# Kernel tuning notes

Measured on AMD Instinct MI355X. Metric: run time of the kernel, lower is better.

The kernel has to match this reference:

```python
import jax, jax.numpy as jnp
import numpy as np

EMBED_DIM = 1024
N_HEADS = 16
HEAD_DIM = EMBED_DIM // N_HEADS


def setup_inputs() -> dict:
    key = jax.random.key(0)
    ks = jax.random.split(key, 9)
    s = 1.0 / np.sqrt(EMBED_DIM)
    x = jax.random.normal(ks[0], (4, 2048, EMBED_DIM), dtype=jnp.float32)
    Wq = jax.random.uniform(ks[1], (EMBED_DIM, EMBED_DIM), jnp.float32, -s, s)
    bq = jax.random.uniform(ks[2], (EMBED_DIM,), jnp.float32, -s, s)
    Wk = jax.random.uniform(ks[3], (EMBED_DIM, EMBED_DIM), jnp.float32, -s, s)
    bk = jax.random.uniform(ks[4], (EMBED_DIM,), jnp.float32, -s, s)
    Wv = jax.random.uniform(ks[5], (EMBED_DIM, EMBED_DIM), jnp.float32, -s, s)
    bv = jax.random.uniform(ks[6], (EMBED_DIM,), jnp.float32, -s, s)
    Wo = jax.random.uniform(ks[7], (EMBED_DIM, EMBED_DIM), jnp.float32, -s, s)
    bo = jax.random.uniform(ks[8], (EMBED_DIM,), jnp.float32, -s, s)
    return {"x": x, "Wq": Wq, "bq": bq, "Wk": Wk, "bk": bk,
            "Wv": Wv, "bv": bv, "Wo": Wo, "bo": bo}


def reference(x, Wq, bq, Wk, bk, Wv, bv, Wo, bo):
    B, S, _ = x.shape
    # projections (PyTorch Linear: x @ W.T + b; weights stored as [in,out] here)
    q = x @ Wq + bq
    k = x @ Wk + bk
    v = x @ Wv + bv
    # [B, H, S, D]
    q = q.reshape(B, S, N_HEADS, HEAD_DIM).transpose(0, 2, 1, 3)
    k = k.reshape(B, S, N_HEADS, HEAD_DIM).transpose(0, 2, 1, 3)
    v = v.reshape(B, S, N_HEADS, HEAD_DIM).transpose(0, 2, 1, 3)
    scores = jnp.einsum('bhsd,bhtd->bhst', q, k) / np.sqrt(HEAD_DIM).astype(np.float32)
    attn = jax.nn.softmax(scores, axis=-1)
    out = jnp.einsum('bhst,bhtd->bhsd', attn, v)
    out = out.transpose(0, 2, 1, 3).reshape(B, S, EMBED_DIM)
    return out @ Wo + bo  # dropout=0 (eval) -> identity
```

## Files before the change

### kernel.cpp

```cpp
#include <hip/hip_runtime.h>
#include <stdint.h>

#define EMBED 1024
#define NH 16
#define HD 64
#define SEQ 2048
#define BATCH 4
#define M_TOT (BATCH*SEQ)
#define QSCALE 0.18033688011112042f

typedef __attribute__((ext_vector_type(8))) short short8;
typedef __attribute__((ext_vector_type(4))) float floatx4;
typedef __attribute__((ext_vector_type(4))) unsigned int uintx4;

__device__ __forceinline__ unsigned short f2bf(float f) {
    union { float f; unsigned int u; } v; v.f = f;
    unsigned int r = v.u + 0x7fffu + ((v.u >> 16) & 1u);
    return (unsigned short)(r >> 16);
}

__device__ __forceinline__ void load_lds16(const unsigned short* g, unsigned short* l) {
    __builtin_amdgcn_global_load_lds(
        (const __attribute__((address_space(1))) unsigned int*)g,
        (__attribute__((address_space(3))) unsigned int*)l, 16, 0, 0);
}

__global__ void cvt_x(const float* __restrict__ x, unsigned short* __restrict__ xb) {
    int i = (blockIdx.x * 256 + threadIdx.x) * 4;
    float4 v = *(const float4*)(x + i);
    ushort4 o;
    o.x = f2bf(v.x); o.y = f2bf(v.y); o.z = f2bf(v.z); o.w = f2bf(v.w);
    *(ushort4*)(xb + i) = o;
}

__global__ void wtrans(const float* __restrict__ w0, const float* __restrict__ w1,
                       const float* __restrict__ w2, const float* __restrict__ w3,
                       unsigned short* __restrict__ t0, unsigned short* __restrict__ t1,
                       unsigned short* __restrict__ t2, unsigned short* __restrict__ t3) {
    __shared__ float tile[32][33];
    const float* W; unsigned short* T;
    switch (blockIdx.z) { case 0: W=w0; T=t0; break; case 1: W=w1; T=t1; break;
                          case 2: W=w2; T=t2; break; default: W=w3; T=t3; }
    int n0 = blockIdx.x * 32, k0 = blockIdx.y * 32;
    int tx = threadIdx.x, ty = threadIdx.y;
    #pragma unroll
    for (int i = 0; i < 4; i++)
        tile[ty + i*8][tx] = W[(k0 + ty + i*8) * EMBED + n0 + tx];
    __syncthreads();
    #pragma unroll
    for (int i = 0; i < 4; i++)
        T[(n0 + ty + i*8) * EMBED + k0 + tx] = f2bf(tile[tx][ty + i*8]);
}

#define GBUFS 8192

template<bool STG, int WAITN>
__device__ __forceinline__ void ktile(int t,
        const unsigned short* Abase, const unsigned short* Bbase,
        const unsigned short* Asrc, const unsigned short* Bsrc,
        unsigned short* sda, unsigned short* sdb, floatx4 (&acc)[4][2]) {
    const int bo = (t & 3) * GBUFS;
    short8 fA[4], fB[2];
    #pragma unroll
    for (int m=0;m<4;m++) fA[m] = *(const short8*)(Abase + bo + m*512);
    #pragma unroll
    for (int n=0;n<2;n++) fB[n] = *(const short8*)(Bbase + bo + n*512);
    if (STG) {
        const int buf_ = (t+3) & 3; const int ko_ = (t+3)*32;
        load_lds16(Asrc + ko_, sda + buf_*GBUFS);
        load_lds16(Bsrc + ko_, sdb + buf_*GBUFS);
    }
    #pragma unroll
    for (int m=0;m<4;m++)
      #pragma unroll
      for (int n=0;n<2;n++)
        acc[m][n] = __builtin_amdgcn_mfma_f32_16x16x32_bf16(fA[m], fB[n], acc[m][n], 0,0,0);
    if (WAITN == 4)      { asm volatile("s_waitcnt vmcnt(4)" ::: "memory"); asm volatile("s_barrier" ::: "memory"); }
    else if (WAITN == 2) { asm volatile("s_waitcnt vmcnt(2)" ::: "memory"); asm volatile("s_barrier" ::: "memory"); }
    else if (WAITN == 0) { asm volatile("s_waitcnt vmcnt(0)" ::: "memory"); asm volatile("s_barrier" ::: "memory"); }
}

template<int MODE>
__global__ __launch_bounds__(512, 4) void gemmk(
        const unsigned short* __restrict__ A, const unsigned short* __restrict__ BT,
        const float* __restrict__ b0, const float* __restrict__ b1, const float* __restrict__ b2,
        void* __restrict__ o0, void* __restrict__ o1, void* __restrict__ o2) {
    constexpr int BM = 128, BN = 128;
    __shared__ unsigned short lds[4*GBUFS];
    const int tid = threadIdx.x;
    const int lane = tid & 63, wave = tid >> 6;
    const int quad = lane >> 4, l16 = lane & 15;
    const int wm = wave >> 2, wn = wave & 3;
    const int id = blockIdx.x;
    constexpr int MS = (M_TOT/BM)/8;
    const int xcd = id & 7, j = id >> 3;
    const int mblk = (xcd * MS + (j % MS)) * BM;
    const int nblk = (j / MS) * BN;

    const int srow = tid >> 2;
    const int scol = ((tid & 3) ^ (srow & 3) ^ ((srow >> 2) & 3)) * 8;
    const unsigned short* Asrc = A  + (size_t)(mblk + srow) * EMBED + scol;
    const unsigned short* Bsrc = BT + (size_t)(nblk + srow) * EMBED + scol;
    unsigned short* sda = lds + wave * 512;
    unsigned short* sdb = lds + BM*32 + wave * 512;

    const int cs = (quad ^ (l16 & 3) ^ ((l16 >> 2) & 3)) * 8;
    const unsigned short* Abase = lds + (wm*64 + l16)*32 + cs;
    const unsigned short* Bbase = lds + BM*32 + (wn*32 + l16)*32 + cs;

    floatx4 acc[4][2];
    #pragma unroll
    for (int m=0;m<4;m++)
      #pragma unroll
      for (int n=0;n<2;n++) acc[m][n] = (floatx4){0.f,0.f,0.f,0.f};

    #pragma unroll
    for (int p=0;p<3;p++) {
        load_lds16(Asrc + p*32, sda + p*GBUFS);
        load_lds16(Bsrc + p*32, sdb + p*GBUFS);
    }
    asm volatile("s_waitcnt vmcnt(4)" ::: "memory");
    asm volatile("s_barrier" ::: "memory");

    #pragma unroll 4
    for (int t = 0; t < 28; ++t)
        ktile<true,4>(t, Abase, Bbase, Asrc, Bsrc, sda, sdb, acc);
    ktile<true, 4>(28, Abase, Bbase, Asrc, Bsrc, sda, sdb, acc);
    ktile<false,2>(29, Abase, Bbase, Asrc, Bsrc, sda, sdb, acc);
    ktile<false,0>(30, Abase, Bbase, Asrc, Bsrc, sda, sdb, acc);
    ktile<false,-1>(31, Abase, Bbase, Asrc, Bsrc, sda, sdb, acc);

    if constexpr (MODE == 1) {
        float* O = (float*)o0;
        #pragma unroll
        for (int mt=0;mt<4;mt++)
          #pragma unroll
          for (int nt=0;nt<2;nt++) {
            int col = nblk + wn*32 + nt*16 + l16;
            float bv = b0[col];
            #pragma unroll
            for (int r=0;r<4;r++) {
                int row = mblk + wm*64 + mt*16 + quad*4 + r;
                O[(size_t)row * EMBED + col] = acc[mt][nt][r] + bv;
            }
          }
    } else {
        int which = nblk >> 10;
        const float* bs = (which==0) ? b0 : (which==1) ? b1 : b2;
        if (which < 2) {
            unsigned short* O = (unsigned short*)((which==0) ? o0 : o1);
            float sc = (which==0) ? QSCALE : 1.f;
            #pragma unroll
            for (int mt=0;mt<4;mt++)
              #pragma unroll
              for (int nt=0;nt<2;nt++) {
                int coll = (nblk & 1023) + wn*32 + nt*16 + l16;
                float bv = bs[coll];
                int h = coll >> 6, d = coll & 63;
                #pragma unroll
                for (int r=0;r<4;r++) {
                    int row = mblk + wm*64 + mt*16 + quad*4 + r;
                    int b = row >> 11, s = row & 2047;
                    O[((size_t)(b*NH + h)*SEQ + s)*HD + d] = f2bf((acc[mt][nt][r] + bv) * sc);
                }
              }
        } else {
            unsigned short* T = lds;
            unsigned short* OV = (unsigned short*)o2;
            size_t rowbase = ((size_t)((mblk >> 11)*1024 + (nblk & 1023))) * SEQ + (mblk & 2047);
            __syncthreads();
            #pragma unroll
            for (int nt=0;nt<2;nt++) {
                int cloc = wn*32 + nt*16 + l16;
                float bv = bs[(nblk & 1023) + cloc];
                #pragma unroll
                for (int mt=0;mt<4;mt++) {
                    int row0 = wm*64 + mt*16 + quad*4;
                    int sp0 = (row0 & ~31) | (((row0 >> 2) & 3) << 3) | (((row0 >> 4) & 1) << 2);
                    ushort4 w;
                    w.x = f2bf(acc[mt][nt][0] + bv);
                    w.y = f2bf(acc[mt][nt][1] + bv);
                    w.z = f2bf(acc[mt][nt][2] + bv);
                    w.w = f2bf(acc[mt][nt][3] + bv);
                    *(ushort4*)(T + cloc*136 + sp0) = w;
                }
            }
            __syncthreads();
            int s0 = (lane & 15) * 8, dloc = lane >> 4;
            #pragma unroll
            for (int i=0;i<4;i++) {
                int c = wave*16 + i*4 + dloc;
                short8 v = *(const short8*)(T + c*136 + s0);
                *(short8*)(OV + rowbase + (size_t)c * SEQ + s0) = v;
            }
        }
    }
}

__global__ __launch_bounds__(512, 4) void attn(
    const unsigned short* __restrict__ Q, const unsigned short* __restrict__ K,
    const unsigned short* __restrict__ VTp, unsigned short* __restrict__ O) {
    __shared__ unsigned short kv[2][8192];
    unsigned short* kvf = &kv[0][0];
    int tid = threadIdx.x;
    int lane = tid & 63, wave = tid >> 6;
    int quad = lane >> 4, l16 = lane & 15;
    int id = blockIdx.x;
    int bh = (id & 7) * 8 + (id >> 6);
    int qblk = (id >> 3) & 7;
    int b = bh >> 4, h = bh & 15;
    int q0 = qblk * 256 + wave * 32;
    const unsigned short* Qb = Q + (size_t)bh * SEQ * HD;
    const unsigned short* Kb = K + (size_t)bh * SEQ * HD;
    const unsigned short* Vb = VTp + (size_t)bh * HD * SEQ;
    int wk = wave & 3, lrow = lane >> 3, lslot = lane & 7;
    const unsigned short *src0, *src1;
    int dst0, dst1, src_step;
    {
        int c0 = wk*2, c1 = wk*2 + 1;
        int r0 = c0*8 + lrow, r1 = c1*8 + lrow;
        int sc = (lslot ^ lrow) * 8;
        if (wave < 4) {
            src0 = Kb + (size_t)r0 * HD + sc;
            src1 = Kb + (size_t)r1 * HD + sc;
            dst0 = c0*512; dst1 = c1*512;
            src_step = 64 * HD;
        } else {
            src0 = Vb + (size_t)r0 * SEQ + sc;
            src1 = Vb + (size_t)r1 * SEQ + sc;
            dst0 = 4096 + c0*512; dst1 = 4096 + c1*512;
            src_step = 64;
        }
    }
    short8 qf[2][2];
    #pragma unroll
    for (int mt=0;mt<2;mt++) {
        const unsigned short* qp = Qb + (size_t)(q0 + mt*16 + l16) * HD + quad*8;
        qf[mt][0] = *(const short8*)(qp);
        qf[mt][1] = *(const short8*)(qp + 32);
    }
    floatx4 o_acc[2][4], l_acc[2];
    #pragma unroll
    for (int mt=0;mt<2;mt++) {
        l_acc[mt] = (floatx4){0.f,0.f,0.f,0.f};
        #pragma unroll
        for (int dt=0;dt<4;dt++) o_acc[mt][dt] = (floatx4){0.f,0.f,0.f,0.f};
    }
    short8 ones;
    #pragma unroll
    for (int jj=0;jj<8;jj++) ones[jj] = (short)0x3F80;
    int koff[4][2], voff[4][2];
    #pragma unroll
    for (int nt=0;nt<4;nt++) {
        int t = nt*16 + l16;
        #pragma unroll
        for (int hh=0;hh<2;hh++)
            koff[nt][hh] = t*64 + ((hh*4 + quad) ^ (t & 7)) * 8;
    }
    #pragma unroll
    for (int dt=0;dt<4;dt++) {
        int d = dt*16 + l16;
        #pragma unroll
        for (int g=0;g<2;g++)
            voff[dt][g] = 4096 + d*64 + ((g*4 + quad) ^ (d & 7)) * 8;
    }

    load_lds16(src0, kvf + dst0);
    load_lds16(src1, kvf + dst1);
    src0 += src_step; src1 += src_step;

    for (int it = 0; it < 32; ++it) {
        const unsigned short* kb = kvf + (it & 1) * 8192;
        if (it < 31) {
            int bo = ((it & 1) ^ 1) * 8192;
            load_lds16(src0, kvf + bo + dst0);
            load_lds16(src1, kvf + bo + dst1);
            src0 += src_step; src1 += src_step;
            asm volatile("s_waitcnt vmcnt(2)" ::: "memory");
        } else {
            asm volatile("s_waitcnt vmcnt(0)" ::: "memory");
        }
        __builtin_amdgcn_s_barrier();
        asm volatile("" ::: "memory");
        floatx4 sacc[4][2];
        __builtin_amdgcn_s_setprio(1);
        #pragma unroll
        for (int nt=0;nt<4;nt++) {
            short8 kf0 = *(const short8*)(kb + koff[nt][0]);
            short8 kf1 = *(const short8*)(kb + koff[nt][1]);
            #pragma unroll
            for (int mt=0;mt<2;mt++) {
                floatx4 s = (floatx4){0.f,0.f,0.f,0.f};
                s = __builtin_amdgcn_mfma_f32_16x16x32_bf16(kf0, qf[mt][0], s, 0, 0, 0);
                s = __builtin_amdgcn_mfma_f32_16x16x32_bf16(kf1, qf[mt][1], s, 0, 0, 0);
                sacc[nt][mt] = s;
            }
        }
        __builtin_amdgcn_s_setprio(0);
        short8 pf[2][2];
        #pragma unroll
        for (int mt=0;mt<2;mt++)
          #pragma unroll
          for (int g=0;g<2;g++) {
            uintx4 pu;
            #pragma unroll
            for (int jp=0;jp<4;jp++) {
                int nt = g*2 + (jp >> 1), rp = (jp & 1) * 2;
                float e0 = __builtin_amdgcn_exp2f(sacc[nt][mt][rp]);
                float e1 = __builtin_amdgcn_exp2f(sacc[nt][mt][rp+1]);
                unsigned int w;
                asm("v_cvt_pk_bf16_f32 %0, %1, %2" : "=v"(w) : "v"(e0), "v"(e1));
                pu[jp] = w;
            }
            pf[mt][g] = __builtin_bit_cast(short8, pu);
          }
        __builtin_amdgcn_s_setprio(1);
        #pragma unroll
        for (int mt=0;mt<2;mt++) {
            l_acc[mt] = __builtin_amdgcn_mfma_f32_16x16x32_bf16(ones, pf[mt][0], l_acc[mt], 0, 0, 0);
            l_acc[mt] = __builtin_amdgcn_mfma_f32_16x16x32_bf16(ones, pf[mt][1], l_acc[mt], 0, 0, 0);
        }
        #pragma unroll
        for (int dt=0;dt<4;dt++)
          #pragma unroll
          for (int g=0;g<2;g++) {
            short8 vf = *(const short8*)(kb + voff[dt][g]);
            #pragma unroll
            for (int mt=0;mt<2;mt++)
                o_acc[mt][dt] = __builtin_amdgcn_mfma_f32_16x16x32_bf16(vf, pf[mt][g], o_acc[mt][dt], 0, 0, 0);
          }
        __builtin_amdgcn_s_setprio(0);
        asm volatile("" ::: "memory");
        __builtin_amdgcn_s_barrier();
    }
    #pragma unroll
    for (int mt=0;mt<2;mt++) {
        float inv = 1.f / l_acc[mt][0];
        int s = q0 + mt*16 + l16;
        #pragma unroll
        for (int dt=0;dt<4;dt++) {
            ushort4 w;
            w.x = f2bf(o_acc[mt][dt][0]*inv);
            w.y = f2bf(o_acc[mt][dt][1]*inv);
            w.z = f2bf(o_acc[mt][dt][2]*inv);
            w.w = f2bf(o_acc[mt][dt][3]*inv);
            *(ushort4*)(O + ((size_t)b*SEQ + s)*EMBED + h*HD + dt*16 + quad*4) = w;
        }
    }
}

extern "C" void kernel_launch(void* const* d_in, const int* in_sizes, int n_in,
                              void* d_out, int out_size, void* d_ws, size_t ws_size,
                              hipStream_t stream) {
    const float* x  = (const float*)d_in[0];
    const float* Wq = (const float*)d_in[1]; const float* bq = (const float*)d_in[2];
    const float* Wk = (const float*)d_in[3]; const float* bk = (const float*)d_in[4];
    const float* Wv = (const float*)d_in[5]; const float* bv = (const float*)d_in[6];
    const float* Wo = (const float*)d_in[7]; const float* bo = (const float*)d_in[8];
    char* ws = (char*)d_ws;
    unsigned short* xb  = (unsigned short*)(ws);
    unsigned short* WqT = (unsigned short*)(ws + (16ull<<20));
    unsigned short* WkT = (unsigned short*)(ws + (18ull<<20));
    unsigned short* WvT = (unsigned short*)(ws + (20ull<<20));
    unsigned short* WoT = (unsigned short*)(ws + (22ull<<20));
    unsigned short* Qb  = (unsigned short*)(ws + (24ull<<20));
    unsigned short* Kb  = (unsigned short*)(ws + (40ull<<20));
    unsigned short* VTb = (unsigned short*)(ws + (56ull<<20));
    unsigned short* Ob  = xb;

    cvt_x<<<(M_TOT*EMBED)/1024, 256, 0, stream>>>(x, xb);
    wtrans<<<dim3(32,32,4), dim3(32,8), 0, stream>>>(Wq,Wk,Wv,Wo, WqT,WkT,WvT,WoT);
    gemmk<0><<<dim3(1536), 512, 0, stream>>>(xb, WqT, bq, bk, bv, Qb, Kb, VTb);
    attn<<<dim3(512), 512, 0, stream>>>(Qb, Kb, VTb, Ob);
    gemmk<1><<<dim3(512), 512, 0, stream>>>(Ob, WoT, bo, bo, bo, (float*)d_out, nullptr, nullptr);
}
```

Measured before the change: 260.2 us.

## Use 256x128 tiles with triple-buffered LDS for the QKV projection GEMM

Adds a dedicated QKV projection kernel in which each block computes a 256x128 output tile, so each wave holds 8x2 MFMA accumulators instead of 4x2. The LDS pipeline moves from four stages to three, and the grid drops from 1536 to 768 blocks. The goal is to load each B tile once per twice as many A rows, which raises arithmetic intensity and cuts global and LDS traffic per FLOP. The cost is higher register pressure, fewer blocks to fill the GPU, and a shallower prefetch pipeline. The output-projection GEMM is cut down to a non-templated kernel holding only the fp32 epilogue.

```diff
diff --git a/kernel.cpp b/kernel.cpp
--- a/kernel.cpp
+++ b/kernel.cpp
@@ -52,6 +52,131 @@
         T[(n0 + ty + i*8) * EMBED + k0 + tx] = f2bf(tile[tx][ty + i*8]);
 }
 
+#define G2BUFS 12288
+
+template<bool STG, int WAITN>
+__device__ __forceinline__ void ktile2(int t,
+        const unsigned short* Abase, const unsigned short* Bbase,
+        const unsigned short* Asrc, const unsigned short* Bsrc,
+        unsigned short* sda, unsigned short* sdb, floatx4 (&acc)[8][2]) {
+    const int bo = (t % 3) * G2BUFS;
+    short8 fA[8], fB[2];
+    #pragma unroll
+    for (int m=0;m<8;m++) fA[m] = *(const short8*)(Abase + bo + m*512);
+    #pragma unroll
+    for (int n=0;n<2;n++) fB[n] = *(const short8*)(Bbase + bo + n*512);
+    if (STG) {
+        const int buf_ = (t+2) % 3; const int ko_ = (t+2)*32;
+        load_lds16(Asrc + ko_,             sda + buf_*G2BUFS);
+        load_lds16(Asrc + 128*EMBED + ko_, sda + buf_*G2BUFS + 4096);
+        load_lds16(Bsrc + ko_,             sdb + buf_*G2BUFS);
+    }
+    #pragma unroll
+    for (int m=0;m<8;m++)
+      #pragma unroll
+      for (int n=0;n<2;n++)
+        acc[m][n] = __builtin_amdgcn_mfma_f32_16x16x32_bf16(fA[m], fB[n], acc[m][n], 0,0,0);
+    if (WAITN == 3)      { asm volatile("s_waitcnt vmcnt(3)" ::: "memory"); asm volatile("s_barrier" ::: "memory"); }
+    else if (WAITN == 0) { asm volatile("s_waitcnt vmcnt(0)" ::: "memory"); asm volatile("s_barrier" ::: "memory"); }
+}
+
+__global__ __launch_bounds__(512, 4) void gemm256(
+        const unsigned short* __restrict__ A, const unsigned short* __restrict__ BT,
+        const float* __restrict__ b0, const float* __restrict__ b1, const float* __restrict__ b2,
+        void* __restrict__ o0, void* __restrict__ o1, void* __restrict__ o2) {
+    __shared__ unsigned short lds[3*G2BUFS];
+    const int tid = threadIdx.x;
+    const int lane = tid & 63, wave = tid >> 6;
+    const int quad = lane >> 4, l16 = lane & 15;
+    const int wm = wave >> 2, wn = wave & 3;
+    const int id = blockIdx.x;
+    const int xcd = id & 7, j = id >> 3;
+    const int mblk = (xcd * 4 + (j & 3)) * 256;
+    const int nblk = (j >> 2) * 128;
+
+    const int srow = tid >> 2;
+    const int scol = ((tid & 3) ^ (srow & 3) ^ ((srow >> 2) & 3)) * 8;
+    const unsigned short* Asrc = A  + (size_t)(mblk + srow) * EMBED + scol;
+    const unsigned short* Bsrc = BT + (size_t)(nblk + srow) * EMBED + scol;
+    unsigned short* sda = lds + wave * 512;
+    unsigned short* sdb = lds + 8192 + wave * 512;
+
+    const int cs = (quad ^ (l16 & 3) ^ ((l16 >> 2) & 3)) * 8;
+    const unsigned short* Abase = lds + (wm*128 + l16)*32 + cs;
+    const unsigned short* Bbase = lds + 8192 + (wn*32 + l16)*32 + cs;
+
+    floatx4 acc[8][2];
+    #pragma unroll
+    for (int m=0;m<8;m++)
+      #pragma unroll
+      for (int n=0;n<2;n++) acc[m][n] = (floatx4){0.f,0.f,0.f,0.f};
+
+    #pragma unroll
+    for (int p=0;p<2;p++) {
+        load_lds16(Asrc + p*32,             sda + p*G2BUFS);
+        load_lds16(Asrc + 128*EMBED + p*32, sda + p*G2BUFS + 4096);
+        load_lds16(Bsrc + p*32,             sdb + p*G2BUFS);
+    }
+    asm volatile("s_waitcnt vmcnt(3)" ::: "memory");
+    asm volatile("s_barrier" ::: "memory");
+
+    #pragma unroll 3
+    for (int t = 0; t < 30; ++t)
+        ktile2<true,3>(t, Abase, Bbase, Asrc, Bsrc, sda, sdb, acc);
+    ktile2<false,0>(30, Abase, Bbase, Asrc, Bsrc, sda, sdb, acc);
+    ktile2<false,-1>(31, Abase, Bbase, Asrc, Bsrc, sda, sdb, acc);
+
+    int which = nblk >> 10;
+    const float* bs = (which==0) ? b0 : (which==1) ? b1 : b2;
+    if (which < 2) {
+        unsigned short* O = (unsigned short*)((which==0) ? o0 : o1);
+        float sc = (which==0) ? QSCALE : 1.f;
+        #pragma unroll
+        for (int mt=0;mt<8;mt++)
+          #pragma unroll
+          for (int nt=0;nt<2;nt++) {
+            int coll = (nblk & 1023) + wn*32 + nt*16 + l16;
+            float bv = bs[coll];
+            int h = coll >> 6, d = coll & 63;
+            #pragma unroll
+            for (int r=0;r<4;r++) {
+                int row = mblk + wm*128 + mt*16 + quad*4 + r;
+                int b = row >> 11, s = row & 2047;
+                O[((size_t)(b*NH + h)*SEQ + s)*HD + d] = f2bf((acc[mt][nt][r] + bv) * sc);
+            }
+          }
+    } else {
+        unsigned short* T = lds;
+        unsigned short* OV = (unsigned short*)o2;
+        size_t rowbase = ((size_t)((mblk >> 11)*1024 + (nblk & 1023))) * SEQ + (mblk & 2047);
+        __syncthreads();
+        #pragma unroll
+        for (int nt=0;nt<2;nt++) {
+            int cloc = wn*32 + nt*16 + l16;
+            float bv = bs[(nblk & 1023) + cloc];
+            #pragma unroll
+            for (int mt=0;mt<8;mt++) {
+                int row0 = wm*128 + mt*16 + quad*4;
+                int sp0 = (row0 & ~31) | (((row0 >> 2) & 3) << 3) | (((row0 >> 4) & 1) << 2);
+                ushort4 w;
+                w.x = f2bf(acc[mt][nt][0] + bv);
+                w.y = f2bf(acc[mt][nt][1] + bv);
+                w.z = f2bf(acc[mt][nt][2] + bv);
+                w.w = f2bf(acc[mt][nt][3] + bv);
+                *(ushort4*)(T + cloc*264 + sp0) = w;
+            }
+        }
+        __syncthreads();
+        int s0 = (lane & 31) * 8, dloc = lane >> 5;
+        #pragma unroll
+        for (int i=0;i<8;i++) {
+            int c = wave*16 + i*2 + dloc;
+            short8 v = *(const short8*)(T + c*264 + s0);
+            *(short8*)(OV + rowbase + (size_t)c * SEQ + s0) = v;
+        }
+    }
+}
+
 #define GBUFS 8192
 
 template<bool STG, int WAITN>
@@ -80,11 +205,9 @@
     else if (WAITN == 0) { asm volatile("s_waitcnt vmcnt(0)" ::: "memory"); asm volatile("s_barrier" ::: "memory"); }
 }
 
-template<int MODE>
 __global__ __launch_bounds__(512, 4) void gemmk(
         const unsigned short* __restrict__ A, const unsigned short* __restrict__ BT,
-        const float* __restrict__ b0, const float* __restrict__ b1, const float* __restrict__ b2,
-        void* __restrict__ o0, void* __restrict__ o1, void* __restrict__ o2) {
+        const float* __restrict__ b0, float* __restrict__ O) {
     constexpr int BM = 128, BN = 128;
     __shared__ unsigned short lds[4*GBUFS];
     const int tid = threadIdx.x;
@@ -130,71 +253,18 @@
     ktile<false,0>(30, Abase, Bbase, Asrc, Bsrc, sda, sdb, acc);
     ktile<false,-1>(31, Abase, Bbase, Asrc, Bsrc, sda, sdb, acc);
 
-    if constexpr (MODE == 1) {
-        float* O = (float*)o0;
-        #pragma unroll
-        for (int mt=0;mt<4;mt++)
-          #pragma unroll
-          for (int nt=0;nt<2;nt++) {
-            int col = nblk + wn*32 + nt*16 + l16;
-            float bv = b0[col];
-            #pragma unroll
-            for (int r=0;r<4;r++) {
-                int row = mblk + wm*64 + mt*16 + quad*4 + r;
-                O[(size_t)row * EMBED + col] = acc[mt][nt][r] + bv;
-            }
-          }
-    } else {
-        int which = nblk >> 10;
-        const float* bs = (which==0) ? b0 : (which==1) ? b1 : b2;
-        if (which < 2) {
-            unsigned short* O = (unsigned short*)((which==0) ? o0 : o1);
-            float sc = (which==0) ? QSCALE : 1.f;
-            #pragma unroll
-            for (int mt=0;mt<4;mt++)
-              #pragma unroll
-              for (int nt=0;nt<2;nt++) {
-                int coll = (nblk & 1023) + wn*32 + nt*16 + l16;
-                float bv = bs[coll];
-                int h = coll >> 6, d = coll & 63;
-                #pragma unroll
-                for (int r=0;r<4;r++) {
-                    int row = mblk + wm*64 + mt*16 + quad*4 + r;
-                    int b = row >> 11, s = row & 2047;
-                    O[((size_t)(b*NH + h)*SEQ + s)*HD + d] = f2bf((acc[mt][nt][r] + bv) * sc);
-                }
-              }
-        } else {
-            unsigned short* T = lds;
-            unsigned short* OV = (unsigned short*)o2;
-            size_t rowbase = ((size_t)((mblk >> 11)*1024 + (nblk & 1023))) * SEQ + (mblk & 2047);
-            __syncthreads();
-            #pragma unroll
-            for (int nt=0;nt<2;nt++) {
-                int cloc = wn*32 + nt*16 + l16;
-                float bv = bs[(nblk & 1023) + cloc];
-                #pragma unroll
-                for (int mt=0;mt<4;mt++) {
-                    int row0 = wm*64 + mt*16 + quad*4;
-                    int sp0 = (row0 & ~31) | (((row0 >> 2) & 3) << 3) | (((row0 >> 4) & 1) << 2);
-                    ushort4 w;
-                    w.x = f2bf(acc[mt][nt][0] + bv);
-                    w.y = f2bf(acc[mt][nt][1] + bv);
-                    w.z = f2bf(acc[mt][nt][2] + bv);
-                    w.w = f2bf(acc[mt][nt][3] + bv);
-                    *(ushort4*)(T + cloc*136 + sp0) = w;
-                }
-            }
-            __syncthreads();
-            int s0 = (lane & 15) * 8, dloc = lane >> 4;
-            #pragma unroll
-            for (int i=0;i<4;i++) {
-                int c = wave*16 + i*4 + dloc;
-                short8 v = *(const short8*)(T + c*136 + s0);
-                *(short8*)(OV + rowbase + (size_t)c * SEQ + s0) = v;
-            }
-        }
-    }
+    #pragma unroll
+    for (int mt=0;mt<4;mt++)
+      #pragma unroll
+      for (int nt=0;nt<2;nt++) {
+        int col = nblk + wn*32 + nt*16 + l16;
+        float bv = b0[col];
+        #pragma unroll
+        for (int r=0;r<4;r++) {
+            int row = mblk + wm*64 + mt*16 + quad*4 + r;
+            O[(size_t)row * EMBED + col] = acc[mt][nt][r] + bv;
+        }
+      }
 }
 
 __global__ __launch_bounds__(512, 4) void attn(
@@ -370,7 +440,7 @@
 
     cvt_x<<<(M_TOT*EMBED)/1024, 256, 0, stream>>>(x, xb);
     wtrans<<<dim3(32,32,4), dim3(32,8), 0, stream>>>(Wq,Wk,Wv,Wo, WqT,WkT,WvT,WoT);
-    gemmk<0><<<dim3(1536), 512, 0, stream>>>(xb, WqT, bq, bk, bv, Qb, Kb, VTb);
+    gemm256<<<dim3(768), 512, 0, stream>>>(xb, WqT, bq, bk, bv, Qb, Kb, VTb);
     attn<<<dim3(512), 512, 0, stream>>>(Qb, Kb, VTb, Ob);
-    gemmk<1><<<dim3(512), 512, 0, stream>>>(Ob, WoT, bo, bo, bo, (float*)d_out, nullptr, nullptr);
-}
+    gemmk<<<dim3(512), 512, 0, stream>>>(Ob, WoT, bo, (float*)d_out);
+}
```

New measurement: 250.8 us. 1.04x faster.
